# Performance work log

Hardware: AMD Instinct MI355X
Metric: run time of the kernel (lower is better)

The kernel has to match this reference:

```python
import jax, jax.numpy as jnp
import numpy as np

POS_IOU_THR = 0.7
NEG_IOU_THR = 0.3
MIN_POS_IOU = 0.3
MATCH_LOW_QUALITY = True

N_BOXES = 500000
N_GTS = 128
DIM = 3  # 3D boxes -> 6 coords


def _make_boxes(key, n, max_size):
    k1, k2 = jax.random.split(key)
    lt = jax.random.uniform(k1, (n, DIM)) * (1.0 - max_size)
    sz = jax.random.uniform(k2, (n, DIM)) * max_size + 1e-3
    return jnp.concatenate([lt, lt + sz], axis=-1)  # [n, 2*DIM], valid lt < rb


def setup_inputs() -> dict:
    key = jax.random.key(0)
    kb, kg, kl = jax.random.split(key, 3)
    bboxes = _make_boxes(kb, N_BOXES, 0.15)
    gt_bboxes = _make_boxes(kg, N_GTS, 0.15)
    gt_labels = jax.random.randint(kl, (N_GTS,), 1, 21, dtype=jnp.int32)
    return {"bboxes": bboxes, "gt_bboxes": gt_bboxes, "gt_labels": gt_labels}


def _iou_nd(b1, b2):
    # b1: [N, 2d], b2: [M, 2d] -> [N, M] axis-aligned IoU in d dims
    d = b1.shape[-1] // 2
    lt = jnp.maximum(b1[:, None, :d], b2[None, :, :d])   # [N, M, d]
    rb = jnp.minimum(b1[:, None, d:], b2[None, :, d:])
    inter = jnp.prod(jnp.clip(rb - lt, 0.0), axis=-1)    # [N, M]
    a1 = jnp.prod(b1[:, d:] - b1[:, :d], axis=-1)        # [N]
    a2 = jnp.prod(b2[:, d:] - b2[:, :d], axis=-1)        # [M]
    return inter / (a1[:, None] + a2[None, :] - inter + 1e-7)


def reference(bboxes, gt_bboxes, gt_labels):
    num_bboxes, num_gts = bboxes.shape[0], gt_bboxes.shape[0]
    iou = _iou_nd(bboxes, gt_bboxes)                      # [N, M]

    anchors_iou_max = jnp.max(iou, axis=1)                # [N]
    anchors_iou_argmax = jnp.argmax(iou, axis=1)          # [N]
    gt_iou_max = jnp.max(iou, axis=0)                     # [M]
    gt_iou_argmax = jnp.argmax(iou, axis=0)               # [M]

    # -1 ignore, 0 negative, n>0 matched gt (1-based)
    assigned = jnp.full((num_bboxes,), -1, dtype=jnp.int32)
    assigned = jnp.where(anchors_iou_max < NEG_IOU_THR, 0, assigned)
    assigned = jnp.where(anchors_iou_max >= POS_IOU_THR,
                         anchors_iou_argmax.astype(jnp.int32) + 1, assigned)

    if MATCH_LOW_QUALITY:
        # torch loop: for i in range(M): if gt_iou_max[i] >= min_pos_iou:
        cand = jnp.where(gt_iou_max >= MIN_POS_IOU,
                         jnp.arange(1, num_gts + 1, dtype=jnp.int32), 0)
        override = jnp.zeros((num_bboxes,), dtype=jnp.int32).at[gt_iou_argmax].max(cand)
        assigned = jnp.where(override > 0, override, assigned)

    pos_mask = assigned > 0
    gi = jnp.clip(assigned - 1, 0)                        # safe gather index
    assigned_labels = jnp.where(pos_mask, gt_labels[gi],
                                jnp.where(assigned == 0, 0, -1)).astype(jnp.int32)
    assigned_bboxes = jnp.where(pos_mask[:, None], gt_bboxes[gi],
                                jnp.full_like(bboxes, -1.0))
    return assigned_labels, assigned_bboxes
```

## Files before the change

### kernel.cpp

```cpp
#include <hip/hip_runtime.h>


#define MMAX 128

#define IOU_ONE(GLO, GHI, G, X0, Y0, Z0, X1, Y1, Z1, AR, BEST, ARG, ENC)       \
    {                                                                          \
        float cx = fmaxf(__fsub_rn(fminf(X1, GLO.w), fmaxf(X0, GLO.x)), 0.f);  \
        float cy = fmaxf(__fsub_rn(fminf(Y1, GHI.x), fmaxf(Y0, GLO.y)), 0.f);  \
        float cz = fmaxf(__fsub_rn(fminf(Z1, GHI.y), fmaxf(Z0, GLO.z)), 0.f);  \
        float inter = __fmul_rn(__fmul_rn(cx, cy), cz);                        \
        if (inter > 0.f) {                                 \
            float den = __fadd_rn(__fsub_rn(__fadd_rn(AR, GHI.z), inter), 1e-7f);\
            float iou = __fdiv_rn(inter, den);                                 \
            if (iou > BEST) { BEST = iou; ARG = (G); }                         \
            if (iou >= 0.3f) {                                                 \
                unsigned long long enc =                                       \
                    ((unsigned long long)__float_as_uint(iou) << 32) |         \
                    (unsigned long long)(ENC);                                 \
                atomicMax(&lsl[(G)], enc);                                     \
            }                                                                  \
        }                                                                      \
    }

#define IOU_G(GLO, GHI, G)                                                     \
    IOU_ONE(GLO, GHI, G, ax0, ay0, az0, ax1, ay1, az1, a1a, bestA, argA, encA) \
    IOU_ONE(GLO, GHI, G, bx0, by0, bz0, bx1, by1, bz1, a1b, bestB, argB, encB) \
    IOU_ONE(GLO, GHI, G, cx0, cy0, cz0, cx1, cy1, cz1, a1c, bestC, argC, encC) \
    IOU_ONE(GLO, GHI, G, dx0, dy0, dz0, dx1, dy1, dz1, a1d, bestD, argD, encD)

template <int MC>
__global__ __launch_bounds__(256) void iou_main(
    const float* __restrict__ bx, const float* __restrict__ gt,
    const int* __restrict__ gl,
    float* __restrict__ out_lab, float* __restrict__ out_bb,
    unsigned long long* __restrict__ slots,
    int N, int Mrt)
{
    const int M = MC ? MC : Mrt;
    const int tid  = threadIdx.x;
    const int lane = tid & 63;
    const int wv   = tid >> 6;

    __shared__ float4 gb4[MMAX * 2];
    __shared__ unsigned long long lsl[MMAX];
    __shared__ unsigned long long asl[256];
    if (tid < M) {
        const float* gp = gt + (size_t)tid * 6;
        float x0 = gp[0], y0 = gp[1], z0 = gp[2];
        float x1 = gp[3], y1 = gp[4], z1 = gp[5];
        float area = __fmul_rn(__fmul_rn(__fsub_rn(x1, x0), __fsub_rn(y1, y0)),
                               __fsub_rn(z1, z0));
        gb4[2 * tid]     = make_float4(x0, y0, z0, x1);
        gb4[2 * tid + 1] = make_float4(y1, z1, area, (float)gl[tid]);
    }
    if (tid < MMAX) lsl[tid] = 0ULL;
    asl[tid] = 0ULL;
    __syncthreads();

    const int H = (N + 3) >> 2;
    const int base = blockIdx.x * 64 + lane;
    const int a = base, b = base + H, c = base + 2 * H, d = base + 3 * H;
    const bool va = (base < H);
    const bool vb = va && (b < N);
    const bool vc = va && (c < N);
    const bool vd = va && (d < N);

    float ax0 = 0.f, ay0 = 0.f, az0 = 0.f, ax1 = 0.f, ay1 = 0.f, az1 = 0.f;
    if (va) { const float* p = bx + (size_t)a * 6;
        ax0 = p[0]; ay0 = p[1]; az0 = p[2]; ax1 = p[3]; ay1 = p[4]; az1 = p[5]; }
    float bx0 = 0.f, by0 = 0.f, bz0 = 0.f, bx1 = 0.f, by1 = 0.f, bz1 = 0.f;
    if (vb) { const float* p = bx + (size_t)b * 6;
        bx0 = p[0]; by0 = p[1]; bz0 = p[2]; bx1 = p[3]; by1 = p[4]; bz1 = p[5]; }
    float cx0 = 0.f, cy0 = 0.f, cz0 = 0.f, cx1 = 0.f, cy1 = 0.f, cz1 = 0.f;
    if (vc) { const float* p = bx + (size_t)c * 6;
        cx0 = p[0]; cy0 = p[1]; cz0 = p[2]; cx1 = p[3]; cy1 = p[4]; cz1 = p[5]; }
    float dx0 = 0.f, dy0 = 0.f, dz0 = 0.f, dx1 = 0.f, dy1 = 0.f, dz1 = 0.f;
    if (vd) { const float* p = bx + (size_t)d * 6;
        dx0 = p[0]; dy0 = p[1]; dz0 = p[2]; dx1 = p[3]; dy1 = p[4]; dz1 = p[5]; }

    const float a1a = __fmul_rn(__fmul_rn(__fsub_rn(ax1, ax0),
                       __fsub_rn(ay1, ay0)), __fsub_rn(az1, az0));
    const float a1b = __fmul_rn(__fmul_rn(__fsub_rn(bx1, bx0),
                       __fsub_rn(by1, by0)), __fsub_rn(bz1, bz0));
    const float a1c = __fmul_rn(__fmul_rn(__fsub_rn(cx1, cx0),
                       __fsub_rn(cy1, cy0)), __fsub_rn(cz1, cz0));
    const float a1d = __fmul_rn(__fmul_rn(__fsub_rn(dx1, dx0),
                       __fsub_rn(dy1, dy0)), __fsub_rn(dz1, dz0));

    const unsigned encA = 0xFFFFFFFFu - (unsigned)a;
    const unsigned encB = 0xFFFFFFFFu - (unsigned)b;
    const unsigned encC = 0xFFFFFFFFu - (unsigned)c;
    const unsigned encD = 0xFFFFFFFFu - (unsigned)d;

    const int chunk = (M + 3) >> 2;
    const int g0 = wv * chunk;
    const int g1 = (g0 + chunk < M) ? (g0 + chunk) : M;

    float bestA = 0.f, bestB = 0.f, bestC = 0.f, bestD = 0.f;
    int   argA = g0,   argB = g0,   argC = g0,   argD = g0;

    int g = g0;
    for (; g + 3 < g1; g += 4) {
        const float4 glo0 = gb4[2*g+0], ghi0 = gb4[2*g+1];
        const float4 glo1 = gb4[2*g+2], ghi1 = gb4[2*g+3];
        const float4 glo2 = gb4[2*g+4], ghi2 = gb4[2*g+5];
        const float4 glo3 = gb4[2*g+6], ghi3 = gb4[2*g+7];
        IOU_G(glo0, ghi0, g + 0)
        IOU_G(glo1, ghi1, g + 1)
        IOU_G(glo2, ghi2, g + 2)
        IOU_G(glo3, ghi3, g + 3)
    }
    for (; g < g1; ++g) {
        const float4 glo = gb4[2*g], ghi = gb4[2*g+1];
        IOU_G(glo, ghi, g)
    }

    if (va) atomicMax(&asl[0 * 64 + lane],
        ((unsigned long long)__float_as_uint(bestA) << 32) |
        (unsigned long long)(0xFFFFFFFFu - (unsigned)argA));
    if (vb) atomicMax(&asl[1 * 64 + lane],
        ((unsigned long long)__float_as_uint(bestB) << 32) |
        (unsigned long long)(0xFFFFFFFFu - (unsigned)argB));
    if (vc) atomicMax(&asl[2 * 64 + lane],
        ((unsigned long long)__float_as_uint(bestC) << 32) |
        (unsigned long long)(0xFFFFFFFFu - (unsigned)argC));
    if (vd) atomicMax(&asl[3 * 64 + lane],
        ((unsigned long long)__float_as_uint(bestD) << 32) |
        (unsigned long long)(0xFFFFFFFFu - (unsigned)argD));
    __syncthreads();

    if (tid < M) {
        unsigned long long v = lsl[tid];
        if (v) atomicMax(&slots[tid], v);
    }

    {
        const int k = tid >> 6, l = tid & 63;
        const int sb = blockIdx.x * 64 + l;
        const int anchor = sb + k * H;
        if (sb < H && anchor < N) {
            const unsigned long long v = asl[tid];
            const float best = __uint_as_float((unsigned)(v >> 32));
            const int garg = (int)(0xFFFFFFFFu - (unsigned)(v & 0xFFFFFFFFu));
            const float* gbf = (const float*)gb4;
            float lab;
            if (best >= 0.7f) lab = gbf[8 * garg + 7];
            else              lab = (best < 0.3f) ? 0.f : -1.f;
            out_lab[anchor] = lab;
            float* ob = out_bb + (size_t)anchor * 6;
            if (best >= 0.7f) {
                ob[0] = gbf[8*garg+0]; ob[1] = gbf[8*garg+1]; ob[2] = gbf[8*garg+2];
                ob[3] = gbf[8*garg+3]; ob[4] = gbf[8*garg+4]; ob[5] = gbf[8*garg+5];
            } else {
                ob[0] = -1.f; ob[1] = -1.f; ob[2] = -1.f;
                ob[3] = -1.f; ob[4] = -1.f; ob[5] = -1.f;
            }
        }
    }
}

__global__ __launch_bounds__(MMAX) void iou_override(
    const float* __restrict__ gt, const int* __restrict__ gl,
    const unsigned long long* __restrict__ slots,
    float* __restrict__ out_lab, float* __restrict__ out_bb, int M)
{
    __shared__ int s_anchor[MMAX];
    __shared__ int s_cand[MMAX];
    const int i = threadIdx.x;

    int anchor = -1, cand = 0;
    if (i < M) {
        unsigned long long v = slots[i];
        if (v != 0ULL) {
            anchor = (int)(0xFFFFFFFFu - (unsigned)(v & 0xFFFFFFFFu));
            cand   = i + 1;
        }
    }
    s_anchor[i] = anchor;
    s_cand[i]   = cand;
    __syncthreads();

    if (cand > 0) {
        bool win = true;
        for (int j = 0; j < M; ++j)
            if (s_cand[j] > cand && s_anchor[j] == anchor) { win = false; break; }
        if (win) {
            out_lab[anchor] = (float)gl[i];
            float* ob = out_bb + (size_t)anchor * 6;
            const float* gp = gt + (size_t)i * 6;
            ob[0] = gp[0]; ob[1] = gp[1]; ob[2] = gp[2];
            ob[3] = gp[3]; ob[4] = gp[4]; ob[5] = gp[5];
        }
    }
}

extern "C" void kernel_launch(void* const* d_in, const int* in_sizes, int n_in,
                              void* d_out, int out_size, void* d_ws, size_t ws_size,
                              hipStream_t stream)
{
    const float* bx = (const float*)d_in[0];
    const float* gt = (const float*)d_in[1];
    const int*   gl = (const int*)d_in[2];
    const int N = in_sizes[0] / 6;
    int M = in_sizes[1] / 6;
    if (M > MMAX) M = MMAX;

    float* out_lab = (float*)d_out;
    float* out_bb  = (float*)d_out + N;

    unsigned long long* slots = (unsigned long long*)d_ws;

    hipMemsetAsync(d_ws, 0, MMAX * 8, stream);

    const int H = (N + 3) / 4;
    const int nblocks = (H + 63) / 64;

    if (M == MMAX) {
        hipLaunchKernelGGL(iou_main<MMAX>, dim3(nblocks), dim3(256), 0, stream,
                           bx, gt, gl, out_lab, out_bb, slots, N, M);
    } else {
        hipLaunchKernelGGL(iou_main<0>, dim3(nblocks), dim3(256), 0, stream,
                           bx, gt, gl, out_lab, out_bb, slots, N, M);
    }
    hipLaunchKernelGGL(iou_override, dim3(1), dim3(MMAX), 0, stream,
                       gt, gl, slots, out_lab, out_bb, M);
}
```

Baseline: 64.02 us.

## Fuse main and override passes into one cooperative persistent kernel

Replaces the memset plus main kernel plus single-block override kernel with one cooperative kernel. It uses a persistent grid-stride loop, writes per-block low-quality slots instead of global atomics, reduces them per GT after a grid sync, and applies the overrides after a second grid sync. This removes launch overhead, the memset and contended global atomicMax. In exchange it adds two grid-wide barriers, per-block slot writes, and a reduction over about 2000 entries for each GT. It also queries occupancy and device attributes on the host on every call.

```diff
diff --git a/kernel.cpp b/kernel.cpp
--- a/kernel.cpp
+++ b/kernel.cpp
@@ -1,4 +1,7 @@
 #include <hip/hip_runtime.h>
+#include <hip/hip_cooperative_groups.h>
+
+namespace cg = cooperative_groups;
 
 
 #define MMAX 128
@@ -29,7 +32,193 @@
     IOU_ONE(GLO, GHI, G, dx0, dy0, dz0, dx1, dy1, dz1, a1d, bestD, argD, encD)
 
 template <int MC>
-__global__ __launch_bounds__(256) void iou_main(
+__global__ __launch_bounds__(256) void iou_fused(
+    const float* __restrict__ bx, const float* __restrict__ gt,
+    const int* __restrict__ gl,
+    float* __restrict__ out_lab, float* __restrict__ out_bb,
+    unsigned long long* __restrict__ slotsPB,
+    unsigned long long* __restrict__ slotRed,
+    int N, int Mrt, int nb)
+{
+    const int M = MC ? MC : Mrt;
+    const int tid  = threadIdx.x;
+    const int lane = tid & 63;
+    const int wv   = tid >> 6;
+
+    __shared__ float4 gb4[MMAX * 2];
+    __shared__ unsigned long long lsl[MMAX];
+    __shared__ unsigned long long asl[256];
+    __shared__ int s_anchor[MMAX];
+    __shared__ int s_cand[MMAX];
+
+    if (tid < M) {
+        const float* gp = gt + (size_t)tid * 6;
+        float x0 = gp[0], y0 = gp[1], z0 = gp[2];
+        float x1 = gp[3], y1 = gp[4], z1 = gp[5];
+        float area = __fmul_rn(__fmul_rn(__fsub_rn(x1, x0), __fsub_rn(y1, y0)),
+                               __fsub_rn(z1, z0));
+        gb4[2 * tid]     = make_float4(x0, y0, z0, x1);
+        gb4[2 * tid + 1] = make_float4(y1, z1, area, (float)gl[tid]);
+    }
+
+    const int H = (N + 3) >> 2;
+    const int chunk = (M + 3) >> 2;
+
+    for (int bid = blockIdx.x; (bid << 6) < H; bid += gridDim.x) {
+        __syncthreads();
+        if (tid < MMAX) lsl[tid] = 0ULL;
+        asl[tid] = 0ULL;
+        __syncthreads();
+
+        const int base = bid * 64 + lane;
+        const int a = base, b = base + H, c = base + 2 * H, d = base + 3 * H;
+        const bool va = (base < H);
+        const bool vb = va && (b < N);
+        const bool vc = va && (c < N);
+        const bool vd = va && (d < N);
+
+        float ax0 = 0.f, ay0 = 0.f, az0 = 0.f, ax1 = 0.f, ay1 = 0.f, az1 = 0.f;
+        if (va) { const float* p = bx + (size_t)a * 6;
+            ax0 = p[0]; ay0 = p[1]; az0 = p[2]; ax1 = p[3]; ay1 = p[4]; az1 = p[5]; }
+        float bx0 = 0.f, by0 = 0.f, bz0 = 0.f, bx1 = 0.f, by1 = 0.f, bz1 = 0.f;
+        if (vb) { const float* p = bx + (size_t)b * 6;
+            bx0 = p[0]; by0 = p[1]; bz0 = p[2]; bx1 = p[3]; by1 = p[4]; bz1 = p[5]; }
+        float cx0 = 0.f, cy0 = 0.f, cz0 = 0.f, cx1 = 0.f, cy1 = 0.f, cz1 = 0.f;
+        if (vc) { const float* p = bx + (size_t)c * 6;
+            cx0 = p[0]; cy0 = p[1]; cz0 = p[2]; cx1 = p[3]; cy1 = p[4]; cz1 = p[5]; }
+        float dx0 = 0.f, dy0 = 0.f, dz0 = 0.f, dx1 = 0.f, dy1 = 0.f, dz1 = 0.f;
+        if (vd) { const float* p = bx + (size_t)d * 6;
+            dx0 = p[0]; dy0 = p[1]; dz0 = p[2]; dx1 = p[3]; dy1 = p[4]; dz1 = p[5]; }
+
+        const float a1a = __fmul_rn(__fmul_rn(__fsub_rn(ax1, ax0),
+                           __fsub_rn(ay1, ay0)), __fsub_rn(az1, az0));
+        const float a1b = __fmul_rn(__fmul_rn(__fsub_rn(bx1, bx0),
+                           __fsub_rn(by1, by0)), __fsub_rn(bz1, bz0));
+        const float a1c = __fmul_rn(__fmul_rn(__fsub_rn(cx1, cx0),
+                           __fsub_rn(cy1, cy0)), __fsub_rn(cz1, cz0));
+        const float a1d = __fmul_rn(__fmul_rn(__fsub_rn(dx1, dx0),
+                           __fsub_rn(dy1, dy0)), __fsub_rn(dz1, dz0));
+
+        const unsigned encA = 0xFFFFFFFFu - (unsigned)a;
+        const unsigned encB = 0xFFFFFFFFu - (unsigned)b;
+        const unsigned encC = 0xFFFFFFFFu - (unsigned)c;
+        const unsigned encD = 0xFFFFFFFFu - (unsigned)d;
+
+        const int g0 = wv * chunk;
+        const int g1 = (g0 + chunk < M) ? (g0 + chunk) : M;
+
+        float bestA = 0.f, bestB = 0.f, bestC = 0.f, bestD = 0.f;
+        int   argA = g0,   argB = g0,   argC = g0,   argD = g0;
+
+        int g = g0;
+        for (; g + 3 < g1; g += 4) {
+            const float4 glo0 = gb4[2*g+0], ghi0 = gb4[2*g+1];
+            const float4 glo1 = gb4[2*g+2], ghi1 = gb4[2*g+3];
+            const float4 glo2 = gb4[2*g+4], ghi2 = gb4[2*g+5];
+            const float4 glo3 = gb4[2*g+6], ghi3 = gb4[2*g+7];
+            IOU_G(glo0, ghi0, g + 0)
+            IOU_G(glo1, ghi1, g + 1)
+            IOU_G(glo2, ghi2, g + 2)
+            IOU_G(glo3, ghi3, g + 3)
+        }
+        for (; g < g1; ++g) {
+            const float4 glo = gb4[2*g], ghi = gb4[2*g+1];
+            IOU_G(glo, ghi, g)
+        }
+
+        if (va) atomicMax(&asl[0 * 64 + lane],
+            ((unsigned long long)__float_as_uint(bestA) << 32) |
+            (unsigned long long)(0xFFFFFFFFu - (unsigned)argA));
+        if (vb) atomicMax(&asl[1 * 64 + lane],
+            ((unsigned long long)__float_as_uint(bestB) << 32) |
+            (unsigned long long)(0xFFFFFFFFu - (unsigned)argB));
+        if (vc) atomicMax(&asl[2 * 64 + lane],
+            ((unsigned long long)__float_as_uint(bestC) << 32) |
+            (unsigned long long)(0xFFFFFFFFu - (unsigned)argC));
+        if (vd) atomicMax(&asl[3 * 64 + lane],
+            ((unsigned long long)__float_as_uint(bestD) << 32) |
+            (unsigned long long)(0xFFFFFFFFu - (unsigned)argD));
+        __syncthreads();
+
+        if (tid < MMAX) slotsPB[(size_t)bid * MMAX + tid] = (tid < M) ? lsl[tid] : 0ULL;
+
+        {
+            const int k = tid >> 6, l = tid & 63;
+            const int sb = bid * 64 + l;
+            const int anchor = sb + k * H;
+            if (sb < H && anchor < N) {
+                const unsigned long long v = asl[tid];
+                const float best = __uint_as_float((unsigned)(v >> 32));
+                const int garg = (int)(0xFFFFFFFFu - (unsigned)(v & 0xFFFFFFFFu));
+                const float* gbf = (const float*)gb4;
+                float lab;
+                if (best >= 0.7f) lab = gbf[8 * garg + 7];
+                else              lab = (best < 0.3f) ? 0.f : -1.f;
+                out_lab[anchor] = lab;
+                float* ob = out_bb + (size_t)anchor * 6;
+                if (best >= 0.7f) {
+                    ob[0] = gbf[8*garg+0]; ob[1] = gbf[8*garg+1]; ob[2] = gbf[8*garg+2];
+                    ob[3] = gbf[8*garg+3]; ob[4] = gbf[8*garg+4]; ob[5] = gbf[8*garg+5];
+                } else {
+                    ob[0] = -1.f; ob[1] = -1.f; ob[2] = -1.f;
+                    ob[3] = -1.f; ob[4] = -1.f; ob[5] = -1.f;
+                }
+            }
+        }
+    }
+
+    cg::this_grid().sync();
+
+    if (blockIdx.x < MMAX) {
+        const int g = blockIdx.x;
+        unsigned long long best = 0ULL;
+        for (int t = tid; t < nb; t += 256) {
+            unsigned long long v = slotsPB[(size_t)t * MMAX + g];
+            if (v > best) best = v;
+        }
+        asl[tid] = best;
+        __syncthreads();
+        for (int s = 128; s > 0; s >>= 1) {
+            if (tid < s) {
+                unsigned long long o = asl[tid + s];
+                if (o > asl[tid]) asl[tid] = o;
+            }
+            __syncthreads();
+        }
+        if (tid == 0) slotRed[g] = asl[0];
+    }
+
+    cg::this_grid().sync();
+
+    if (blockIdx.x == 0) {
+        int anchor = -1, cand = 0;
+        if (tid < M) {
+            unsigned long long v = slotRed[tid];
+            if (v != 0ULL) {
+                anchor = (int)(0xFFFFFFFFu - (unsigned)(v & 0xFFFFFFFFu));
+                cand   = tid + 1;
+            }
+        }
+        if (tid < MMAX) { s_anchor[tid] = anchor; s_cand[tid] = cand; }
+        __syncthreads();
+        if (tid < M && cand > 0) {
+            bool win = true;
+            for (int j = 0; j < M; ++j)
+                if (s_cand[j] > cand && s_anchor[j] == anchor) win = false;
+            if (win) {
+                const float4 gl4 = gb4[2 * tid], gh4 = gb4[2 * tid + 1];
+                out_lab[anchor] = gh4.w;
+                float* ob = out_bb + (size_t)anchor * 6;
+                ob[0] = gl4.x; ob[1] = gl4.y; ob[2] = gl4.z;
+                ob[3] = gl4.w; ob[4] = gh4.x; ob[5] = gh4.y;
+            }
+        }
+    }
+}
+
+
+template <int MC>
+__global__ __launch_bounds__(256) void iou_main_legacy(
     const float* __restrict__ bx, const float* __restrict__ gt,
     const int* __restrict__ gl,
     float* __restrict__ out_lab, float* __restrict__ out_bb,
@@ -159,7 +348,7 @@
     }
 }
 
-__global__ __launch_bounds__(MMAX) void iou_override(
+__global__ __launch_bounds__(MMAX) void iou_override_legacy(
     const float* __restrict__ gt, const int* __restrict__ gl,
     const unsigned long long* __restrict__ slots,
     float* __restrict__ out_lab, float* __restrict__ out_bb, int M)
@@ -208,20 +397,53 @@
     float* out_lab = (float*)d_out;
     float* out_bb  = (float*)d_out + N;
 
-    unsigned long long* slots = (unsigned long long*)d_ws;
-
-    hipMemsetAsync(d_ws, 0, MMAX * 8, stream);
-
     const int H = (N + 3) / 4;
-    const int nblocks = (H + 63) / 64;
-
-    if (M == MMAX) {
-        hipLaunchKernelGGL(iou_main<MMAX>, dim3(nblocks), dim3(256), 0, stream,
-                           bx, gt, gl, out_lab, out_bb, slots, N, M);
+    const int nb = (H + 63) / 64;
+    const size_t needPB = (size_t)nb * MMAX * 8 + MMAX * 8;
+
+    if (ws_size >= needPB) {
+        unsigned long long* slotsPB = (unsigned long long*)d_ws;
+        unsigned long long* slotRed =
+            (unsigned long long*)((char*)d_ws + (size_t)nb * MMAX * 8);
+
+        int bpc = 0;
+        if (M == MMAX) {
+            hipOccupancyMaxActiveBlocksPerMultiprocessor(
+                &bpc, (const void*)iou_fused<MMAX>, 256, 0);
+        } else {
+            hipOccupancyMaxActiveBlocksPerMultiprocessor(
+                &bpc, (const void*)iou_fused<0>, 256, 0);
+        }
+        if (bpc < 1) bpc = 1;
+        int dev = 0, ncu = 256;
+        hipGetDevice(&dev);
+        hipDeviceGetAttribute(&ncu, hipDeviceAttributeMultiprocessorCount, dev);
+        int grid = bpc * ncu;
+        if (grid > nb) grid = nb;
+        if (grid < MMAX) grid = MMAX;
+
+        void* args[] = { (void*)&bx, (void*)&gt, (void*)&gl,
+                         (void*)&out_lab, (void*)&out_bb,
+                         (void*)&slotsPB, (void*)&slotRed,
+                         (void*)&N, (void*)&M, (void*)&nb };
+        if (M == MMAX) {
+            hipLaunchCooperativeKernel((const void*)iou_fused<MMAX>,
+                                       dim3(grid), dim3(256), args, 0, stream);
+        } else {
+            hipLaunchCooperativeKernel((const void*)iou_fused<0>,
+                                       dim3(grid), dim3(256), args, 0, stream);
+        }
     } else {
-        hipLaunchKernelGGL(iou_main<0>, dim3(nblocks), dim3(256), 0, stream,
-                           bx, gt, gl, out_lab, out_bb, slots, N, M);
-    }
-    hipLaunchKernelGGL(iou_override, dim3(1), dim3(MMAX), 0, stream,
-                       gt, gl, slots, out_lab, out_bb, M);
+        unsigned long long* slots = (unsigned long long*)d_ws;
+        hipMemsetAsync(d_ws, 0, MMAX * 8, stream);
+        if (M == MMAX) {
+            hipLaunchKernelGGL(iou_main_legacy<MMAX>, dim3(nb), dim3(256), 0, stream,
+                               bx, gt, gl, out_lab, out_bb, slots, N, M);
+        } else {
+            hipLaunchKernelGGL(iou_main_legacy<0>, dim3(nb), dim3(256), 0, stream,
+                               bx, gt, gl, out_lab, out_bb, slots, N, M);
+        }
+        hipLaunchKernelGGL(iou_override_legacy, dim3(1), dim3(MMAX), 0, stream,
+                           gt, gl, slots, out_lab, out_bb, M);
+    }
 }
```

Result: slower. 186.9 us (+191.9%).
